# Optimization experiments

Measured on AMD Instinct MI355X. Metric: run time of the kernel, lower is better.

Reference implementation:

```python
import jax, jax.numpy as jnp
import numpy as np

H, D = 8, 8          # num_heads, hidden_size (head dim)
SCALE = 0.25         # Hopfield beta/scaling
STEPS = 3            # update_steps_max
LN_EPS = 1e-5


def ln(x, g, b):
    m = x.mean(-1, keepdims=True)
    v = ((x - m) ** 2).mean(-1, keepdims=True)
    return (x - m) * jax.lax.rsqrt(v + LN_EPS) * g + b


def setup_inputs() -> dict:
    key = jax.random.key(0)
    ks = jax.random.split(key, 8)
    B, N, E = 32, 512, 512
    P = H * D  # 64 virtual hopfield dim
    s = lambda k, shape: jax.random.normal(k, shape, jnp.float32) * 0.05
    return dict(
        x=jax.random.normal(ks[0], (B, N, E), jnp.float32),
        g_q=jnp.ones((E,), jnp.float32), b_q=jnp.zeros((E,), jnp.float32),
        g_k=jnp.ones((E,), jnp.float32), b_k=jnp.zeros((E,), jnp.float32),
        g_v=jnp.ones((E,), jnp.float32), b_v=jnp.zeros((E,), jnp.float32),
        Wq=s(ks[1], (P, E)), bq=jnp.zeros((P,), jnp.float32),
        Wk=s(ks[2], (P, E)), bk=jnp.zeros((P,), jnp.float32),
        Wv=s(ks[3], (P, E)), bv=jnp.zeros((P,), jnp.float32),
        Wo=s(ks[4], (E, P)), bo=jnp.zeros((E,), jnp.float32),
        Wl=s(ks[5], (1, N * E)), bl=jnp.zeros((1,), jnp.float32),
    )


def reference(x, g_q, b_q, g_k, b_k, g_v, b_v,
              Wq, bq, Wk, bk, Wv, bv, Wo, bo, Wl, bl):
    B, N, E = x.shape
    # LayerNorm on state (query), stored (key), projection (value) patterns
    q = (ln(x, g_q, b_q) @ Wq.T + bq).reshape(B, N, H, D)
    k = (ln(x, g_k, b_k) @ Wk.T + bk).reshape(B, N, H, D)
    v = (ln(x, g_v, b_v) @ Wv.T + bv).reshape(B, N, H, D)
    # iterative Hopfield retrieval: xi <- softmax(beta * xi K^T) K
    xi = q
    for _ in range(STEPS):
        a = jax.nn.softmax(SCALE * jnp.einsum('bihd,bjhd->bhij', xi, k), axis=-1)
        xi = jnp.einsum('bhij,bjhd->bihd', a, k)
    # final association with value patterns
    a = jax.nn.softmax(SCALE * jnp.einsum('bihd,bjhd->bhij', xi, k), axis=-1)
    o = jnp.einsum('bhij,bjhd->bihd', a, v).reshape(B, N, H * D)
    o = o @ Wo.T + bo              # (B, N, E) out projection
    y = o.reshape(B, N * E) @ Wl.T + bl  # (B, 1) classifier head
    return y.reshape(-1)           # flatten(start_dim=0) -> (B,)
```

## Files before the change

kernel.cpp:

```cpp
#include <hip/hip_runtime.h>

#define E_DIM 512
#define N_DIM 512
#define B_DIM 32
#define H_DIM 8
#define D_DIM 8
#define P3    192

typedef _Float16 half_t;
typedef __attribute__((ext_vector_type(2))) _Float16 half2v;
typedef __attribute__((ext_vector_type(4))) _Float16 half4v;
typedef __attribute__((ext_vector_type(8))) _Float16 half8v;
typedef __attribute__((ext_vector_type(4))) float f32x4;
typedef __attribute__((ext_vector_type(16))) float f32x16;
typedef __attribute__((ext_vector_type(2))) unsigned int u32x2;
typedef __attribute__((ext_vector_type(4))) unsigned int u32x4;

#define XS_STRIDE 520
#define CQ 0.3606737602222409f

#define SM_KT0 0
#define SM_VT0 4608
#define SM_KB0 9216
#define SM_TOT 13312

__device__ inline float block_reduce_256(float v) {
    __shared__ float red[4];
    #pragma unroll
    for (int m = 32; m >= 1; m >>= 1) v += __shfl_xor(v, m);
    int w = threadIdx.x >> 6;
    if ((threadIdx.x & 63) == 0) red[w] = v;
    __syncthreads();
    if (threadIdx.x == 0) v = red[0] + red[1] + red[2] + red[3];
    return v;
}

__device__ inline half8v cvt8(float4 a, float4 b) {
    half8v h;
    h[0] = (half_t)a.x; h[1] = (half_t)a.y; h[2] = (half_t)a.z; h[3] = (half_t)a.w;
    h[4] = (half_t)b.x; h[5] = (half_t)b.y; h[6] = (half_t)b.z; h[7] = (half_t)b.w;
    return h;
}

__device__ inline unsigned pku(float a, float b) {
    return __builtin_bit_cast(unsigned, __builtin_amdgcn_cvt_pkrtz(a, b));
}

__device__ inline void plswap(unsigned &a, unsigned &b) {
    u32x2 r = __builtin_amdgcn_permlane32_swap(a, b, false, false);
    a = r[0]; b = r[1];
}

__device__ inline float bcast_lo(float v) {
    unsigned u = __builtin_bit_cast(unsigned, v);
    u32x2 r = __builtin_amdgcn_permlane32_swap(u, u, false, false);
    return __builtin_bit_cast(float, r[0]);
}

__global__ __launch_bounds__(256) void prep_w(const float* __restrict__ Wq,
                        const float* __restrict__ Wk, const float* __restrict__ Wv,
                        const float* __restrict__ gq, const float* __restrict__ gk,
                        const float* __restrict__ gv,
                        const float* __restrict__ bnq, const float* __restrict__ bnk,
                        const float* __restrict__ bnv,
                        const float* __restrict__ bq, const float* __restrict__ bk,
                        const float* __restrict__ bv,
                        const float* __restrict__ bl,
                        half_t* __restrict__ WthF, float* __restrict__ colsum,
                        float* __restrict__ b2, float* __restrict__ y,
                        float* __restrict__ c0acc) {
    int pp = blockIdx.x;
    int which = pp >> 6, p = pp & 63;
    int ct = pp >> 4, c16 = pp & 15;
    const float* W  = (which == 0) ? Wq  : (which == 1) ? Wk  : Wv;
    const float* g  = (which == 0) ? gq  : (which == 1) ? gk  : gv;
    const float* bn = (which == 0) ? bnq : (which == 1) ? bnk : bnv;
    const float* bb = (which == 0) ? bq  : (which == 1) ? bk  : bv;
    int t = threadIdx.x;
    if (pp == 0) {
        if (t < 32) y[t] = bl[0];
        if (t == 32) c0acc[0] = 0.f;
    }
    float cs = 0.f, dt = 0.f;
    #pragma unroll
    for (int l = 0; l < 2; ++l) {
        int e = t + l * 256;
        float wv = W[p * E_DIM + e];
        half_t wh = (half_t)(wv * g[e]);
        int k32 = e >> 5, g2 = (e >> 3) & 3, j = e & 7;
        WthF[(((size_t)(ct * 16 + k32) * 64) + g2 * 16 + c16) * 8 + j] = wh;
        cs += (float)wh;
        dt += wv * bn[e];
    }
    cs = block_reduce_256(cs);
    __syncthreads();
    dt = block_reduce_256(dt);
    if (t == 0) { colsum[pp] = cs; b2[pp] = dt + bb[p]; }
}

__global__ __launch_bounds__(256) void ln_qkv_wl2(const float* __restrict__ x,
                                              const half_t* __restrict__ WthF,
                                              const float* __restrict__ b2,
                                              const float* __restrict__ colsum,
                                              half_t* __restrict__ qkv16,
                                              const float* __restrict__ Wl,
                                              const float* __restrict__ Wo,
                                              const float* __restrict__ bo,
                                              float* __restrict__ Wl2,
                                              float* __restrict__ c0acc) {
    __shared__ half_t Xs[16 * XS_STRIDE];
    __shared__ float stats[16][2];
    if (blockIdx.x < 1024) {
        const int t = threadIdx.x;
        const int lane = t & 63;
        const int w = t >> 6;
        const int g2 = lane >> 4, c16 = lane & 15;
        const int row0 = blockIdx.x * 16;
        {
            const int row = t >> 4, c = t & 15;
            const float4* xrow = (const float4*)(x + (size_t)(row0 + row) * E_DIM);
            float sx = 0.f, sxx = 0.f;
            #pragma unroll
            for (int l = 0; l < 8; ++l) {
                int f4 = c + l * 16;
                float4 a = xrow[f4];
                sx  += a.x + a.y + a.z + a.w;
                sxx += a.x*a.x + a.y*a.y + a.z*a.z + a.w*a.w;
                half4v h;
                h[0] = (half_t)a.x; h[1] = (half_t)a.y;
                h[2] = (half_t)a.z; h[3] = (half_t)a.w;
                *(half4v*)&Xs[row * XS_STRIDE + f4 * 4] = h;
            }
            #pragma unroll
            for (int m = 1; m <= 8; m <<= 1) {
                sx += __shfl_xor(sx, m); sxx += __shfl_xor(sxx, m);
            }
            if (c == 0) {
                float mean = sx * (1.f / E_DIM);
                float var  = sxx * (1.f / E_DIM) - mean * mean;
                stats[row][0] = mean;
                stats[row][1] = rsqrtf(var + 1e-5f);
            }
        }
        __syncthreads();
        f32x4 acc[3] = {{0.f,0.f,0.f,0.f},{0.f,0.f,0.f,0.f},{0.f,0.f,0.f,0.f}};
        const half_t* wf = WthF + (size_t)w * 3 * 16 * 512;
        #pragma unroll 4
        for (int k32 = 0; k32 < 16; ++k32) {
            half8v af = *(const half8v*)&Xs[c16 * XS_STRIDE + k32 * 32 + g2 * 8];
            #pragma unroll
            for (int nt = 0; nt < 3; ++nt) {
                half8v bf = *(const half8v*)(wf + ((size_t)(nt * 16 + k32)) * 512 + lane * 8);
                acc[nt] = __builtin_amdgcn_mfma_f32_16x16x32_f16(af, bf, acc[nt], 0, 0, 0);
            }
        }
        #pragma unroll
        for (int nt = 0; nt < 3; ++nt) {
            int pp = w * 48 + nt * 16 + c16;
            float cs = colsum[pp], bb = b2[pp];
            float qsc = (w * 3 + nt < 4) ? CQ : 1.0f;
            int which = pp >> 6, p = pp & 63;
            int h = p >> 3, d = p & 7;
            half_t* dst0 = qkv16 + (size_t)which * (B_DIM * H_DIM * N_DIM * D_DIM);
            #pragma unroll
            for (int r = 0; r < 4; ++r) {
                int rowi = g2 * 4 + r;
                float val = (stats[rowi][1] * (acc[nt][r] - stats[rowi][0] * cs) + bb) * qsc;
                int ng = row0 + rowi;
                int b = ng >> 9, n = ng & 511;
                dst0[(((size_t)(b * H_DIM + h)) * N_DIM + n) * D_DIM + d] = (half_t)val;
            }
        }
    } else {
        const int blk = blockIdx.x - 1024;
        const int t = threadIdx.x;
        const int lane = t & 63;
        const int w = t >> 6;
        const int g2 = lane >> 4, c16 = lane & 15;
        const int n0 = blk * 16;
        const int pcol = w * 16;
        f32x4 acc = {0.f, 0.f, 0.f, 0.f};
        float pc = 0.f;
        const float* arow = Wl + (size_t)(n0 + c16) * E_DIM;
        #pragma unroll 2
        for (int k0 = 0; k0 < E_DIM; k0 += 32) {
            int kbase = k0 + g2 * 8;
            float4 a0 = *(const float4*)(arow + kbase);
            float4 a1 = *(const float4*)(arow + kbase + 4);
            if (w == 0) {
                float4 b0 = *(const float4*)(bo + kbase);
                float4 b1 = *(const float4*)(bo + kbase + 4);
                pc += a0.x*b0.x + a0.y*b0.y + a0.z*b0.z + a0.w*b0.w
                    + a1.x*b1.x + a1.y*b1.y + a1.z*b1.z + a1.w*b1.w;
            }
            half8v af = cvt8(a0, a1);
            half8v bf;
            #pragma unroll
            for (int j = 0; j < 8; ++j)
                bf[j] = (half_t)Wo[(size_t)(kbase + j) * 64 + pcol + c16];
            acc = __builtin_amdgcn_mfma_f32_16x16x32_f16(af, bf, acc, 0, 0, 0);
        }
        int p = pcol + c16, h = p >> 3, d = p & 7;
        #pragma unroll
        for (int r = 0; r < 4; ++r) {
            int n = n0 + g2 * 4 + r;
            Wl2[h * (N_DIM * D_DIM) + n * D_DIM + d] = acc[r];
        }
        if (w == 0) {
            pc += __shfl_xor(pc, 16); pc += __shfl_xor(pc, 32);
            pc += __shfl_xor(pc, 1);  pc += __shfl_xor(pc, 2);
            pc += __shfl_xor(pc, 4);  pc += __shfl_xor(pc, 8);
            if (lane == 0) atomicAdd(c0acc, pc);
        }
    }
}

__global__ __launch_bounds__(256, 4) void hopfield(const half_t* __restrict__ q16,
                                                   const half_t* __restrict__ k16,
                                                   const half_t* __restrict__ v16,
                                                   const float* __restrict__ Wl2,
                                                   const float* __restrict__ c0acc,
                                                   float* __restrict__ y) {
    __shared__ __align__(16) half_t sm[SM_TOT];
    const int t = threadIdx.x;
    const int lane = t & 63;
    const int w = t >> 6;
    const int lq = lane & 31;
    const int hi = lane >> 5;
    const int bh = blockIdx.x >> 2, seg = blockIdx.x & 3;
    const half_t* kg = k16 + (size_t)bh * (N_DIM * D_DIM);
    const half_t* vg = v16 + (size_t)bh * (N_DIM * D_DIM);
    const half_t* qg = q16 + (size_t)bh * (N_DIM * D_DIM) + seg * 128 * 8;
    const float* wl2p = Wl2 + (bh & 7) * (N_DIM * D_DIM) + seg * 128 * 8;

    {
        const int j0 = 2 * t;
        half8v r0 = *(const half8v*)(kg + j0 * 8);
        half8v r1 = *(const half8v*)(kg + j0 * 8 + 8);
        half8v v0 = *(const half8v*)(vg + j0 * 8);
        half8v v1 = *(const half8v*)(vg + j0 * 8 + 8);
        *(half8v*)&sm[SM_KB0 + j0 * 8]     = r0;
        *(half8v*)&sm[SM_KB0 + j0 * 8 + 8] = r1;
        const int kt = t >> 2, jp = j0 & 7;
        half_t* kb = &sm[SM_KT0 + kt * 72 + jp];
        half_t* vb = &sm[SM_VT0 + kt * 72 + jp];
        #pragma unroll
        for (int d = 0; d < 8; ++d) {
            half2v pk_; pk_[0] = r0[d]; pk_[1] = r1[d];
            *(half2v*)(kb + d * 8) = pk_;
            half2v pv_; pv_[0] = v0[d]; pv_[1] = v1[d];
            *(half2v*)(vb + d * 8) = pv_;
        }
        half2v one2; one2[0] = (half_t)1.f; one2[1] = (half_t)1.f;
        *(half2v*)(kb + 64) = one2;
        *(half2v*)(vb + 64) = one2;
    }
    __syncthreads();

    const half_t* akbase = sm + SM_KB0 + (hi ? 0 : lq * 8);
    const int akstep = hi ? 0 : 256;
    int rowc = lq & 15; if (rowc > 8) rowc = 8;
    const half_t* aTk = sm + SM_KT0 + hi * 72 + rowc * 8;
    const f32x16 Zf16 = {};
    float fsum = 0.f;

    half8v bx;
    {
        half8v bq = *(const half8v*)(qg + (w * 32 + lq) * 8);
        u32x4 qw = __builtin_bit_cast(u32x4, bq);
        if (hi) { qw[0] = 0u; qw[1] = 0u; qw[2] = 0u; qw[3] = 0u; }
        bx = __builtin_bit_cast(half8v, qw);
    }

    for (int it = 0; it < 4; ++it) {
        const half_t* aTit = aTk + (it == 3 ? (SM_VT0 - SM_KT0) : 0);
        const half_t* akp = akbase;
        f32x16 U = {};
        for (int tile = 0; tile < 16; ++tile) {
            half8v ak = *(const half8v*)akp;
            akp += akstep;
            half8v aT0 = *(const half8v*)(aTit + tile * 288);
            half8v aT1 = *(const half8v*)(aTit + tile * 288 + 144);
            f32x16 S = __builtin_amdgcn_mfma_f32_32x32x16_f16(ak, bx, Zf16, 0, 0, 0);
            unsigned wa = pku(__builtin_amdgcn_exp2f(S[0]),  __builtin_amdgcn_exp2f(S[1]));
            unsigned wb = pku(__builtin_amdgcn_exp2f(S[2]),  __builtin_amdgcn_exp2f(S[3]));
            unsigned wc = pku(__builtin_amdgcn_exp2f(S[4]),  __builtin_amdgcn_exp2f(S[5]));
            unsigned wd = pku(__builtin_amdgcn_exp2f(S[6]),  __builtin_amdgcn_exp2f(S[7]));
            unsigned we = pku(__builtin_amdgcn_exp2f(S[8]),  __builtin_amdgcn_exp2f(S[9]));
            unsigned wf = pku(__builtin_amdgcn_exp2f(S[10]), __builtin_amdgcn_exp2f(S[11]));
            unsigned wg = pku(__builtin_amdgcn_exp2f(S[12]), __builtin_amdgcn_exp2f(S[13]));
            unsigned wh = pku(__builtin_amdgcn_exp2f(S[14]), __builtin_amdgcn_exp2f(S[15]));
            plswap(wa, wc); plswap(wb, wd);
            plswap(we, wg); plswap(wf, wh);
            u32x4 c0 = {wa, wb, wc, wd};
            u32x4 c1 = {we, wf, wg, wh};
            U = __builtin_amdgcn_mfma_f32_32x32x16_f16(aT0, __builtin_bit_cast(half8v, c0), U, 0, 0, 0);
            U = __builtin_amdgcn_mfma_f32_32x32x16_f16(aT1, __builtin_bit_cast(half8v, c1), U, 0, 0, 0);
        }
        float inv = __builtin_amdgcn_rcpf(bcast_lo(U[4]));
        if (it < 3) {
            float ci = CQ * inv;
            unsigned W01 = pku(U[0] * ci, U[1] * ci);
            unsigned W23 = pku(U[2] * ci, U[3] * ci);
            unsigned z1 = 0u, z2 = 0u;
            plswap(W01, z1);
            plswap(W23, z2);
            u32x4 nb = {W01, W23, z1, z2};
            bx = __builtin_bit_cast(half8v, nb);
        } else {
            float4 wv = *(const float4*)&wl2p[(w * 32 + lq) * 8 + hi * 4];
            fsum = inv * (U[0] * wv.x + U[1] * wv.y + U[2] * wv.z + U[3] * wv.w);
        }
    }
    float tot = block_reduce_256(fsum);
    if (t == 0) atomicAdd(&y[bh >> 3], tot);
    if (blockIdx.x == 0 && t < 32) {
        atomicAdd(&y[t], c0acc[0]);
    }
}

extern "C" void kernel_launch(void* const* d_in, const int* in_sizes, int n_in,
                              void* d_out, int out_size, void* d_ws, size_t ws_size,
                              hipStream_t stream) {
    const float* x   = (const float*)d_in[0];
    const float* g_q = (const float*)d_in[1];
    const float* b_q = (const float*)d_in[2];
    const float* g_k = (const float*)d_in[3];
    const float* b_k = (const float*)d_in[4];
    const float* g_v = (const float*)d_in[5];
    const float* b_v = (const float*)d_in[6];
    const float* Wq  = (const float*)d_in[7];
    const float* bq  = (const float*)d_in[8];
    const float* Wk  = (const float*)d_in[9];
    const float* bk  = (const float*)d_in[10];
    const float* Wv  = (const float*)d_in[11];
    const float* bv  = (const float*)d_in[12];
    const float* Wo  = (const float*)d_in[13];
    const float* bo  = (const float*)d_in[14];
    const float* Wl  = (const float*)d_in[15];
    const float* bl  = (const float*)d_in[16];
    float* out = (float*)d_out;

    float* ws = (float*)d_ws;
    float*  colsum = ws;
    float*  b2     = ws + 192;
    float*  c0acc  = ws + 384;
    float*  Wl2    = ws + 448;
    half_t* WthF   = (half_t*)(ws + 33216);
    half_t* qkv16  = (half_t*)(ws + 82368);

    half_t* q16 = qkv16;
    half_t* k16 = qkv16 + 1048576;
    half_t* v16 = qkv16 + 2097152;

    prep_w    <<<192, 256, 0, stream>>>(Wq, Wk, Wv, g_q, g_k, g_v,
                                        b_q, b_k, b_v, bq, bk, bv, bl,
                                        WthF, colsum, b2, out, c0acc);
    ln_qkv_wl2<<<1056, 256, 0, stream>>>(x, WthF, b2, colsum, qkv16,
                                         Wl, Wo, bo, Wl2, c0acc);
    hopfield  <<<1024, 256, 0, stream>>>(q16, k16, v16, Wl2, c0acc, out);
}
```

Measured before the change: 155.9 us.

## Stage QKV stores through LDS and software-pipeline score MFMA in Hopfield loop

The QKV projection epilogue now writes results into a shared-memory staging buffer and then emits coalesced 4-half vector stores to global memory, replacing scattered 2-byte stores. In the attention loop, the score MFMA for the next tile is issued before the exp2/pack work of the current tile, with s_setprio raised around the softmax-and-accumulate section, so matrix and VALU work can overlap. The hi lanes now load real K rows instead of a broadcast address. This adds LDS usage, an extra barrier and higher register pressure from the live next-tile accumulator.

```diff
diff --git a/kernel.cpp b/kernel.cpp
--- a/kernel.cpp
+++ b/kernel.cpp
@@ -18,6 +18,7 @@
 
 #define XS_STRIDE 520
 #define CQ 0.3606737602222409f
+#define LS_RS 136
 
 #define SM_KT0 0
 #define SM_VT0 4608
@@ -109,6 +110,7 @@
                                               float* __restrict__ Wl2,
                                               float* __restrict__ c0acc) {
     __shared__ half_t Xs[16 * XS_STRIDE];
+    __shared__ half_t Ls[24 * LS_RS];
     __shared__ float stats[16][2];
     if (blockIdx.x < 1024) {
         const int t = threadIdx.x;
@@ -158,18 +160,26 @@
         for (int nt = 0; nt < 3; ++nt) {
             int pp = w * 48 + nt * 16 + c16;
             float cs = colsum[pp], bb = b2[pp];
-            float qsc = (w * 3 + nt < 4) ? CQ : 1.0f;
-            int which = pp >> 6, p = pp & 63;
-            int h = p >> 3, d = p & 7;
-            half_t* dst0 = qkv16 + (size_t)which * (B_DIM * H_DIM * N_DIM * D_DIM);
+            float qsc = (pp < 64) ? CQ : 1.0f;
+            int region = pp >> 3, d = pp & 7;
             #pragma unroll
             for (int r = 0; r < 4; ++r) {
                 int rowi = g2 * 4 + r;
                 float val = (stats[rowi][1] * (acc[nt][r] - stats[rowi][0] * cs) + bb) * qsc;
-                int ng = row0 + rowi;
-                int b = ng >> 9, n = ng & 511;
-                dst0[(((size_t)(b * H_DIM + h)) * N_DIM + n) * D_DIM + d] = (half_t)val;
-            }
+                Ls[region * LS_RS + rowi * 8 + d] = (half_t)val;
+            }
+        }
+        __syncthreads();
+        const int b = row0 >> 9, n0 = row0 & 511;
+        #pragma unroll
+        for (int l = 0; l < 3; ++l) {
+            int c = t + l * 256;
+            int region = c >> 5, off = (c & 31) * 4;
+            int which = region >> 3, h = region & 7;
+            half4v v = *(const half4v*)&Ls[region * LS_RS + off];
+            half_t* dst0 = qkv16 + (size_t)which * (B_DIM * H_DIM * N_DIM * D_DIM);
+            int rowi = off >> 3, d0 = off & 7;
+            *(half4v*)&dst0[(((size_t)(b * H_DIM + h)) * N_DIM + n0 + rowi) * D_DIM + d0] = v;
         }
     } else {
         const int blk = blockIdx.x - 1024;
@@ -257,10 +267,10 @@
     }
     __syncthreads();
 
-    const half_t* akbase = sm + SM_KB0 + (hi ? 0 : lq * 8);
-    const int akstep = hi ? 0 : 256;
+    const half_t* akb = sm + SM_KB0 + lq * 8;
     int rowc = lq & 15; if (rowc > 8) rowc = 8;
     const half_t* aTk = sm + SM_KT0 + hi * 72 + rowc * 8;
+    const half_t* aVk = sm + SM_VT0 + hi * 72 + rowc * 8;
     const f32x16 Zf16 = {};
     float fsum = 0.f;
 
@@ -273,15 +283,20 @@
     }
 
     for (int it = 0; it < 4; ++it) {
-        const half_t* aTit = aTk + (it == 3 ? (SM_VT0 - SM_KT0) : 0);
-        const half_t* akp = akbase;
+        const half_t* aTit = (it == 3) ? aVk : aTk;
         f32x16 U = {};
+        half8v ak0 = *(const half8v*)akb;
+        f32x16 Sn = __builtin_amdgcn_mfma_f32_32x32x16_f16(ak0, bx, Zf16, 0, 0, 0);
+        #pragma unroll 4
         for (int tile = 0; tile < 16; ++tile) {
-            half8v ak = *(const half8v*)akp;
-            akp += akstep;
+            f32x16 S = Sn;
+            if (tile < 15) {
+                half8v akn = *(const half8v*)(akb + (tile + 1) * 256);
+                Sn = __builtin_amdgcn_mfma_f32_32x32x16_f16(akn, bx, Zf16, 0, 0, 0);
+            }
             half8v aT0 = *(const half8v*)(aTit + tile * 288);
             half8v aT1 = *(const half8v*)(aTit + tile * 288 + 144);
-            f32x16 S = __builtin_amdgcn_mfma_f32_32x32x16_f16(ak, bx, Zf16, 0, 0, 0);
+            __builtin_amdgcn_s_setprio(1);
             unsigned wa = pku(__builtin_amdgcn_exp2f(S[0]),  __builtin_amdgcn_exp2f(S[1]));
             unsigned wb = pku(__builtin_amdgcn_exp2f(S[2]),  __builtin_amdgcn_exp2f(S[3]));
             unsigned wc = pku(__builtin_amdgcn_exp2f(S[4]),  __builtin_amdgcn_exp2f(S[5]));
@@ -296,6 +311,7 @@
             u32x4 c1 = {we, wf, wg, wh};
             U = __builtin_amdgcn_mfma_f32_32x32x16_f16(aT0, __builtin_bit_cast(half8v, c0), U, 0, 0, 0);
             U = __builtin_amdgcn_mfma_f32_32x32x16_f16(aT1, __builtin_bit_cast(half8v, c1), U, 0, 0, 0);
+            __builtin_amdgcn_s_setprio(0);
         }
         float inv = __builtin_amdgcn_rcpf(bcast_lo(U[4]));
         if (it < 3) {
```

New measurement: 155.6 us. No clear change (-0.2%).
